# Performance work log

Measured on AMD Instinct MI355X. Metric: run time of the kernel, lower is better.

## Reference

```python
import jax, jax.numpy as jnp
import numpy as np
import math

D_MODEL = 1024
N_HEAD = 16
NUM_K = 170


def setup_inputs() -> dict:
    key = jax.random.key(0)
    ks = jax.random.split(key, 11)
    B, S, D = 2, 1024, D_MODEL
    scale = 1.0 / math.sqrt(D)
    inp = {
        "q": jax.random.normal(ks[0], (B, S, D), dtype=jnp.float32),
        "k": jax.random.normal(ks[1], (B, S, D), dtype=jnp.float32),
        "v": jax.random.normal(ks[2], (B, S, D), dtype=jnp.float32),
        # nn.Linear weights stored torch-style as (out, in); y = x @ W.T + b
        "wq": jax.random.normal(ks[3], (D, D), dtype=jnp.float32) * scale,
        "bq": jnp.zeros((D,), dtype=jnp.float32),
        "wk": jax.random.normal(ks[4], (D, D), dtype=jnp.float32) * scale,
        "bk": jnp.zeros((D,), dtype=jnp.float32),
        "wv": jax.random.normal(ks[5], (D, D), dtype=jnp.float32) * scale,
        "bv": jnp.zeros((D,), dtype=jnp.float32),
        "wo": jax.random.normal(ks[6], (D, D), dtype=jnp.float32) * scale,
        "bo": jnp.zeros((D,), dtype=jnp.float32),
    }
    return inp


def _split_heads(x):
    B, S, D = x.shape
    dh = D // N_HEAD
    return x.reshape(B, S, N_HEAD, dh).transpose(0, 2, 1, 3)  # [B,H,S,dh]


def reference(q, k, v, wq, bq, wk, bk, wv, bv, wo, bo):
    B, S, D = q.shape
    dh = D // N_HEAD
    qh = _split_heads(q @ wq.T + bq)
    kh = _split_heads(k @ wk.T + bk)
    vh = _split_heads(v @ wv.T + bv)
    # full QK^T scores [B,H,S,S]
    score = jnp.einsum("bhqd,bhkd->bhqk", qh, kh) / math.sqrt(dh)
    # topk threshold masking: keep only scores >= k-th largest per row
    num_k = min(NUM_K, S)
    topv = jax.lax.top_k(score, num_k)[0]           # [B,H,S,num_k], sorted desc
    thr = topv[..., -1:]                             # k-th largest value
    score = jnp.where(score < thr, jnp.float32(-1e18), score)
    attn = jax.nn.softmax(score, axis=-1)
    out = jnp.einsum("bhqk,bhkd->bhqd", attn, vh)   # [B,H,S,dh]
    out = out.transpose(0, 2, 1, 3).reshape(B, S, D)
    return out @ wo.T + bo
```

## Files before the change

### kernel.cpp

```cpp
#include <hip/hip_runtime.h>

typedef unsigned short u16;
typedef unsigned int   u32;
typedef short bf16x8 __attribute__((ext_vector_type(8)));
typedef float f32x4  __attribute__((ext_vector_type(4)));
typedef float f32x2  __attribute__((ext_vector_type(2)));

#define MFMA(a,b,c) __builtin_amdgcn_mfma_f32_16x16x32_bf16((a),(b),(c),0,0,0)
#define MB (1u<<20)

__device__ __forceinline__ u16 f2bf(float x) {
  u32 u = __builtin_bit_cast(u32, x);
  u32 r = (u + 0x7FFFu + ((u >> 16) & 1u)) >> 16;
  return (u16)r;
}
__device__ __forceinline__ float bf2f(u16 b) {
  u32 u = ((u32)b) << 16;
  return __builtin_bit_cast(float, u);
}
__device__ __forceinline__ void async16(void* lds, const void* g) {
  __builtin_amdgcn_global_load_lds(
      (const __attribute__((address_space(1))) u32*)g,
      (__attribute__((address_space(3))) u32*)lds, 16, 0, 0);
}


__global__ __launch_bounds__(256) void presplit_kernel(
    const float* q, const float* k, const float* v,
    const float* wq, const float* wk, const float* wv, const float* wo,
    char* ws)
{
  int y = blockIdx.y;
  const float* srcs[7] = {q, k, v, wq, wk, wv, wo};
  size_t hoffv = (y < 3) ? (size_t)y * (8*MB) : (size_t)(24*MB) + (size_t)(y-3) * (4*MB);
  size_t loffv = hoffv + ((y < 3) ? (size_t)(4*MB) : (size_t)(2*MB));
  bool wlo = (y == 0) || (y == 1) || (y == 3) || (y == 4);
  int n = (y < 3) ? (2*1024*1024) : (1024*1024);
  int idx = (blockIdx.x * 256 + threadIdx.x) * 4;
  if (idx >= n) return;
  float4 x = *(const float4*)(srcs[y] + idx);
  ushort4 hv; hv.x = f2bf(x.x); hv.y = f2bf(x.y); hv.z = f2bf(x.z); hv.w = f2bf(x.w);
  *(ushort4*)(ws + hoffv + (size_t)idx * 2) = hv;
  if (wlo) {
    ushort4 lv;
    lv.x = f2bf(x.x - bf2f(hv.x)); lv.y = f2bf(x.y - bf2f(hv.y));
    lv.z = f2bf(x.z - bf2f(hv.z)); lv.w = f2bf(x.w - bf2f(hv.w));
    *(ushort4*)(ws + loffv + (size_t)idx * 2) = lv;
  }
}

#define PA_H 0
#define PA_L 16384
#define PB_H 32768
#define PB_L 49152
#define PROJ_LDS 65536

__global__ __launch_bounds__(512, 4) void proj_kernel(char* ws,
    const float* bq, const float* bk, const float* bv)
{
  __shared__ __align__(16) char smem[PROJ_LDS];
  const int z = blockIdx.y;
  const bool split = (z < 2);
  const u16* Ah = (const u16*)(ws + (size_t)z*(8*MB));
  const u16* Al = (const u16*)(ws + (size_t)z*(8*MB) + 4*MB);
  const u16* Bh = (const u16*)(ws + (size_t)(24*MB) + (size_t)z*(4*MB));
  const u16* Bl = (const u16*)(ws + (size_t)(24*MB) + (size_t)z*(4*MB) + 2*MB);
  u16* Oh = (u16*)(ws + (size_t)(40*MB) + (size_t)z*(8*MB));
  u16* Ol = (u16*)(ws + (size_t)(40*MB) + (size_t)z*(8*MB) + 4*MB);
  const float* bias = (z == 0) ? bq : ((z == 1) ? bk : bv);
  const float scale = (z == 0) ? 0.125f : 1.0f;

  const int t = threadIdx.x, w = t >> 6, lane = t & 63;
  const int l15 = lane & 15, l4 = lane >> 4;
  const int m0 = (blockIdx.x >> 3) * 128;
  const int n0 = (blockIdx.x & 7) * 128;
  const int mw = (w >> 2) * 64, nw = (w & 3) * 32;

  f32x4 acc[4][2];
  const f32x4 z4 = {0.f, 0.f, 0.f, 0.f};
  #pragma unroll
  for (int i = 0; i < 4; ++i)
    #pragma unroll
    for (int j = 0; j < 2; ++j) acc[i][j] = z4;

  for (int kt = 0; kt < 16; ++kt) {
    __syncthreads();
    #pragma unroll
    for (int i = 0; i < 2; ++i) {
      int chunk = w*128 + i*64 + lane;
      int row = chunk >> 3, seg = chunk & 7;
      int ss = seg ^ (row & 7);
      size_t ga = (size_t)(m0 + row) * 1024 + kt*64 + ss*8;
      size_t gb = (size_t)(n0 + row) * 1024 + kt*64 + ss*8;
      async16(smem + PA_H + chunk*16, Ah + ga);
      async16(smem + PB_H + chunk*16, Bh + gb);
      if (split) {
        async16(smem + PA_L + chunk*16, Al + ga);
        async16(smem + PB_L + chunk*16, Bl + gb);
      }
    }
    __syncthreads();
    #pragma unroll
    for (int kf = 0; kf < 2; ++kf) {
      bf16x8 avh[4], avl[4], bvh[2], bvl[2];
      #pragma unroll
      for (int mf = 0; mf < 4; ++mf) {
        int row = mw + mf*16 + l15;
        int ks = kf*4 + l4;
        int off = row*128 + ((ks ^ (row & 7)) << 4);
        avh[mf] = *(const bf16x8*)(smem + PA_H + off);
        if (split) avl[mf] = *(const bf16x8*)(smem + PA_L + off);
      }
      #pragma unroll
      for (int nf = 0; nf < 2; ++nf) {
        int row = nw + nf*16 + l15;
        int ks = kf*4 + l4;
        int off = row*128 + ((ks ^ (row & 7)) << 4);
        bvh[nf] = *(const bf16x8*)(smem + PB_H + off);
        if (split) bvl[nf] = *(const bf16x8*)(smem + PB_L + off);
      }
      #pragma unroll
      for (int mf = 0; mf < 4; ++mf)
        #pragma unroll
        for (int nf = 0; nf < 2; ++nf) {
          acc[mf][nf] = MFMA(avh[mf], bvh[nf], acc[mf][nf]);
          if (split) {
            acc[mf][nf] = MFMA(avh[mf], bvl[nf], acc[mf][nf]);
            acc[mf][nf] = MFMA(avl[mf], bvh[nf], acc[mf][nf]);
          }
        }
    }
  }
  #pragma unroll
  for (int mf = 0; mf < 4; ++mf)
    #pragma unroll
    for (int nf = 0; nf < 2; ++nf) {
      int colg = n0 + nw + nf*16 + l15;
      float bb = bias[colg];
      #pragma unroll
      for (int r = 0; r < 4; ++r) {
        int rowg = m0 + mw + mf*16 + l4*4 + r;
        float val = (acc[mf][nf][r] + bb) * scale;
        u16 hb = f2bf(val);
        if (z == 2) {
          Oh[(size_t)rowg * 1024 + colg] = hb;
        } else {
          int bq_ = rowg >> 10, s = rowg & 1023;
          int hh = colg >> 6, d = colg & 63;
          int bh2 = bq_*16 + hh;
          int reg = d >> 5, l4s = (d & 31) >> 3, de = d & 7;
          int lane2 = l4s*16 + (s & 15);
          size_t o;
          if (z == 0) o = ((size_t)((bh2*64 + (s >> 4))*2 + reg))*512 + lane2*8 + de;
          else        o = ((size_t)(((bh2*8 + (s >> 7))*8 + ((s >> 4) & 7))*2 + reg))*512 + lane2*8 + de;
          Oh[o] = hb;
          Ol[o] = f2bf(val - bf2f(hb));
        }
      }
    }
}

#define FA_H 0
#define FB_H 16384
#define FIN_LDS 24576

__global__ __launch_bounds__(256, 3) void final_kernel(char* ws, const float* bo, float* out)
{
  __shared__ __align__(16) char smem[FIN_LDS];
  const u16* Ah = (const u16*)(ws + (size_t)(8*MB));
  const u16* Bh = (const u16*)(ws + (size_t)(36*MB));
  const int t = threadIdx.x, w = t >> 6, lane = t & 63;
  const int l15 = lane & 15, l4 = lane >> 4;
  const int m0 = (blockIdx.x >> 4) * 128;
  const int n0 = (blockIdx.x & 15) * 64;
  const int mw = (w >> 1) * 64, nw = (w & 1) * 32;

  f32x4 acc[4][2];
  const f32x4 z4 = {0.f, 0.f, 0.f, 0.f};
  #pragma unroll
  for (int i = 0; i < 4; ++i)
    #pragma unroll
    for (int j = 0; j < 2; ++j) acc[i][j] = z4;

  for (int kt = 0; kt < 16; ++kt) {
    __syncthreads();
    #pragma unroll
    for (int i = 0; i < 4; ++i) {
      int chunk = w*256 + i*64 + lane;
      int row = chunk >> 3, seg = chunk & 7;
      int ss = seg ^ (row & 7);
      async16(smem + FA_H + chunk*16, Ah + (size_t)(m0 + row) * 1024 + kt*64 + ss*8);
    }
    #pragma unroll
    for (int i = 0; i < 2; ++i) {
      int chunk = w*128 + i*64 + lane;
      if (chunk < 512) {
        int row = chunk >> 3, seg = chunk & 7;
        int ss = seg ^ (row & 7);
        async16(smem + FB_H + chunk*16, Bh + (size_t)(n0 + row) * 1024 + kt*64 + ss*8);
      }
    }
    __syncthreads();
    #pragma unroll
    for (int kf = 0; kf < 2; ++kf) {
      bf16x8 avh[4], bvh[2];
      #pragma unroll
      for (int mf = 0; mf < 4; ++mf) {
        int row = mw + mf*16 + l15;
        int ks = kf*4 + l4;
        avh[mf] = *(const bf16x8*)(smem + FA_H + row*128 + ((ks ^ (row & 7)) << 4));
      }
      #pragma unroll
      for (int nf = 0; nf < 2; ++nf) {
        int row = nw + nf*16 + l15;
        int ks = kf*4 + l4;
        bvh[nf] = *(const bf16x8*)(smem + FB_H + row*128 + ((ks ^ (row & 7)) << 4));
      }
      #pragma unroll
      for (int mf = 0; mf < 4; ++mf)
        #pragma unroll
        for (int nf = 0; nf < 2; ++nf)
          acc[mf][nf] = MFMA(avh[mf], bvh[nf], acc[mf][nf]);
    }
  }
  #pragma unroll
  for (int mf = 0; mf < 4; ++mf)
    #pragma unroll
    for (int nf = 0; nf < 2; ++nf) {
      int colg = n0 + nw + nf*16 + l15;
      float bb = bo[colg];
      #pragma unroll
      for (int r = 0; r < 4; ++r) {
        int rowg = m0 + mw + mf*16 + l4*4 + r;
        out[(size_t)rowg * 1024 + colg] = acc[mf][nf][r] + bb;
      }
    }
}

__global__ __launch_bounds__(256) void vtrans_kernel(char* ws)
{
  __shared__ u16 th[64][68];
  const u16* Vph = (const u16*)(ws + (size_t)(56*MB));
  u16* Vf = (u16*)(ws + 0);
  int id = blockIdx.x;
  int bh = id >> 4, sc = id & 15;
  int b = bh >> 4, h = bh & 15;
  int t = threadIdx.x;
  #pragma unroll
  for (int j = 0; j < 16; ++j) {
    int e = t + 256*j;
    int sr = e >> 6, dc = e & 63;
    th[sr][dc] = Vph[(size_t)(b*1024 + sc*64 + sr) * 1024 + h*64 + dc];
  }
  __syncthreads();
  #pragma unroll
  for (int j = 0; j < 16; ++j) {
    int e = t + 256*j;
    int dr = e >> 6, scl = e & 63;
    int s = sc*64 + scl;
    int f = dr >> 4, l15v = dr & 15;
    int half = s >> 9, ks = (s >> 5) & 15, l4v = (s >> 3) & 3, de = s & 7;
    size_t o = ((size_t)(((bh*4 + f)*2 + half)*16 + ks))*512 + (l4v*16 + l15v)*8 + de;
    Vf[o] = th[scl][dr];
  }
}

#define CB_STRIDE 528
#define CB_SZ     8448
#define P_STRIDE  2064
#define PART_OFF  33024
#define ATT_LDS   (PART_OFF + 4096)
#define KSEL 170

__global__ __launch_bounds__(512, 6) void attn_kernel(char* ws)
{
  __shared__ __align__(16) char smem[ATT_LDS];
  const u16* Qh  = (const u16*)(ws + (size_t)(40*MB));
  const u16* Ql  = (const u16*)(ws + (size_t)(44*MB));
  const u16* Kh  = (const u16*)(ws + (size_t)(48*MB));
  const u16* Kl  = (const u16*)(ws + (size_t)(52*MB));
  const u16* Vf  = (const u16*)(ws + 0);
  u16* Ath = (u16*)(ws + (size_t)(8*MB));

  int t = threadIdx.x, w = t >> 6, lane = t & 63;
  int l15 = lane & 15, l4 = lane >> 4;
  int bid = blockIdx.x;
  int logical = (bid & 7) * 256 + (bid >> 3);
  int bh = logical >> 6, qt = logical & 63;
  int b = bh >> 4, h = bh & 15;
  int q0 = qt * 16;

  const f32x4 z4 = {0.f, 0.f, 0.f, 0.f};

  bf16x8 kf[4];
#define LOADKC(KC) do { \
    size_t kb2 = ((size_t)(((bh*8 + (KC))*8 + w)*2))*512 + lane*8; \
    kf[0] = *(const bf16x8*)(Kh + kb2); \
    kf[1] = *(const bf16x8*)(Kh + kb2 + 512); \
    kf[2] = *(const bf16x8*)(Kl + kb2); \
    kf[3] = *(const bf16x8*)(Kl + kb2 + 512); \
  } while (0)

  LOADKC(0);

  bf16x8 qfh[2], qfl[2];
  {
    size_t qb2 = ((size_t)((bh*64 + qt)*2))*512 + lane*8;
    qfh[0] = *(const bf16x8*)(Qh + qb2);
    qfh[1] = *(const bf16x8*)(Qh + qb2 + 512);
    qfl[0] = *(const bf16x8*)(Ql + qb2);
    qfl[1] = *(const bf16x8*)(Ql + qb2 + 512);
  }

  f32x2 va[8], vb[8];
  #pragma unroll
  for (int kc = 0; kc < 8; ++kc) {
    f32x4 a0 = z4, a1 = z4;
    a0 = MFMA(qfh[0], kf[0], a0);
    a1 = MFMA(qfh[1], kf[1], a1);
    a0 = MFMA(qfl[0], kf[0], a0);
    a1 = MFMA(qfl[1], kf[1], a1);
    a0 = MFMA(qfh[0], kf[2], a0);
    a1 = MFMA(qfh[1], kf[3], a1);
    if (kc < 7) LOADKC(kc + 1);
    #pragma unroll
    for (int r_ = 0; r_ < 4; ++r_)
      *(float*)(smem + (kc & 1)*CB_SZ + (l4*4 + r_)*CB_STRIDE + (w*16 + l15)*4)
          = a0[r_] + a1[r_];
    asm volatile("s_waitcnt lgkmcnt(0)" ::: "memory");
    __builtin_amdgcn_s_barrier();
    asm volatile("" ::: "memory");
    va[kc] = *(const f32x2*)(smem + (kc & 1)*CB_SZ + w*CB_STRIDE + lane*8);
    vb[kc] = *(const f32x2*)(smem + (kc & 1)*CB_SZ + (w + 8)*CB_STRIDE + lane*8);
  }
  __syncthreads();

  int f = w & 3, half = w >> 2;
  size_t vbase = ((size_t)(((bh*4 + f)*2 + half)*16))*512 + lane*8;
  bf16x8 vv[2][4];
#define LOADV(BUF, G) do { \
    _Pragma("unroll") \
    for (int j_ = 0; j_ < 4; ++j_) \
      vv[BUF][j_] = *(const bf16x8*)(Vf + vbase + (size_t)((G)*4 + j_)*512); \
    } while (0)

  {
    float mA = va[0][0], mB = vb[0][0];
    #pragma unroll
    for (int i = 0; i < 8; ++i)
      #pragma unroll
      for (int e = 0; e < 2; ++e) {
        mA = fmaxf(mA, va[i][e]);
        mB = fmaxf(mB, vb[i][e]);
      }
    #pragma unroll
    for (int off = 32; off > 0; off >>= 1) {
      mA = fmaxf(mA, __shfl_xor(mA, off));
      mB = fmaxf(mB, __shfl_xor(mB, off));
    }

    float loA = mA - 16.f, hiA = mA, cLoA = 1024.f, cHiA = 1.f;
    float loB = mB - 16.f, hiB = mB, cLoB = 1024.f, cHiB = 1.f;
    float thrA = 0.f, thrB = 0.f;
    bool fA = false, fB = false;
    #pragma unroll 1
    for (int it = 0; it < 32 && !(fA && fB); ++it) {
      float gA, gB;
      if (it < 8) {
        gA = fminf(fmaxf((cLoA - (float)KSEL) / fmaxf(cLoA - cHiA, 1.f), 0.10f), 0.90f);
        gB = fminf(fmaxf((cLoB - (float)KSEL) / fmaxf(cLoB - cHiB, 1.f), 0.10f), 0.90f);
      } else {
        gA = 0.5f; gB = 0.5f;
      }
      float tA = loA + (hiA - loA) * gA;
      float tB = loB + (hiB - loB) * gB;
      if (!(tA > loA && tA < hiA)) { if (!fA) { thrA = loA; fA = true; } tA = loA; }
      if (!(tB > loB && tB < hiB)) { if (!fB) { thrB = loB; fB = true; } tB = loB; }
      int cA = 0, cB = 0;
      #pragma unroll
      for (int i = 0; i < 8; ++i)
        #pragma unroll
        for (int e = 0; e < 2; ++e) {
          cA += (int)__popcll(__ballot(va[i][e] >= tA));
          cB += (int)__popcll(__ballot(vb[i][e] >= tB));
        }
      if (!fA) {
        if (cA == KSEL) { thrA = tA; fA = true; }
        else if (cA > KSEL) { loA = tA; cLoA = (float)cA; }
        else { hiA = tA; cHiA = (float)cA; }
      }
      if (!fB) {
        if (cB == KSEL) { thrB = tB; fB = true; }
        else if (cB > KSEL) { loB = tB; cLoB = (float)cB; }
        else { hiB = tB; cHiB = (float)cB; }
      }
    }
    if (!fA) thrA = loA;
    if (!fB) thrB = loB;

    LOADV(0, 0);

    float sA = 0.f, sB = 0.f;
    #pragma unroll
    for (int i = 0; i < 8; ++i)
      #pragma unroll
      for (int e = 0; e < 2; ++e) {
        float xa = va[i][e], xb = vb[i][e];
        float ea = (xa >= thrA) ? __expf(xa - mA) : 0.f;
        float eb = (xb >= thrB) ? __expf(xb - mB) : 0.f;
        va[i][e] = ea; vb[i][e] = eb;
        sA += ea; sB += eb;
      }
    #pragma unroll
    for (int off = 32; off > 0; off >>= 1) {
      sA += __shfl_xor(sA, off);
      sB += __shfl_xor(sB, off);
    }
    float rA_ = 1.f / sA, rB_ = 1.f / sB;

    #pragma unroll
    for (int i = 0; i < 8; ++i) {
      u32 pwA = (u32)f2bf(va[i][0] * rA_) | ((u32)f2bf(va[i][1] * rA_) << 16);
      u32 pwB = (u32)f2bf(vb[i][0] * rB_) | ((u32)f2bf(vb[i][1] * rB_) << 16);
      *(u32*)(smem + w*P_STRIDE       + i*256 + lane*4) = pwA;
      *(u32*)(smem + (w + 8)*P_STRIDE + i*256 + lane*4) = pwB;
    }
  }
  __syncthreads();

  LOADV(1, 1);
  f32x4 ac0 = z4, ac1 = z4;
  #pragma unroll
  for (int g = 0; g < 4; ++g) {
    #pragma unroll
    for (int j = 0; j < 4; ++j) {
      int ksl = g*4 + j;
      bf16x8 pa = *(const bf16x8*)(smem + l15*P_STRIDE + (half*16 + ksl)*64 + l4*16);
      if (j & 1) ac1 = MFMA(pa, vv[g & 1][j], ac1);
      else       ac0 = MFMA(pa, vv[g & 1][j], ac0);
    }
    if (g == 0) LOADV(0, 2);
    if (g == 1) LOADV(1, 3);
  }
  f32x4 a = ac0 + ac1;

  if (half == 1)
    *(f32x4*)(smem + PART_OFF + (f*64 + lane)*16) = a;
  __syncthreads();
  if (half == 0) {
    f32x4 o4 = *(const f32x4*)(smem + PART_OFF + (f*64 + lane)*16);
    #pragma unroll
    for (int r = 0; r < 4; ++r) {
      float val = a[r] + o4[r];
      size_t o = (size_t)(b*1024 + q0 + l4*4 + r) * 1024 + h*64 + f*16 + l15;
      Ath[o] = f2bf(val);
    }
  }
}

extern "C" void kernel_launch(void* const* d_in, const int* in_sizes, int n_in,
                              void* d_out, int out_size, void* d_ws, size_t ws_size,
                              hipStream_t stream)
{
  const float* q  = (const float*)d_in[0];
  const float* k  = (const float*)d_in[1];
  const float* v  = (const float*)d_in[2];
  const float* wq = (const float*)d_in[3];
  const float* bq = (const float*)d_in[4];
  const float* wk = (const float*)d_in[5];
  const float* bk = (const float*)d_in[6];
  const float* wv = (const float*)d_in[7];
  const float* bv = (const float*)d_in[8];
  const float* wo = (const float*)d_in[9];
  const float* bo = (const float*)d_in[10];
  float* out = (float*)d_out;
  char* ws = (char*)d_ws;
  if (ws_size < (64ull << 20)) return;

  presplit_kernel<<<dim3(2048, 7), 256, 0, stream>>>(q, k, v, wq, wk, wv, wo, ws);
  proj_kernel<<<dim3(128, 3), 512, 0, stream>>>(ws, bq, bk, bv);
  vtrans_kernel<<<512, 256, 0, stream>>>(ws);
  attn_kernel<<<2048, 512, 0, stream>>>(ws);
  final_kernel<<<256, 256, 0, stream>>>(ws, bo, out);
}
```

Measured before the change: 138.6 us.

## Interleave projection blocks, shrink final GEMM tiles, and hoist V prefetch

The projection kernel now uses a 1D grid that interleaves the Q/K/V jobs, so the split-precision Q/K tiles and the cheaper V tiles mix across CUs. The final output GEMM switches from 128x64 to 64x64 tiles, doubling the block count to 512 to fill more CUs, at the cost of less operand reuse per block. In the attention kernel, the first two V-fragment loads are issued before the threshold search so their latency overlaps the top-k computation, which keeps more registers live.

```diff
diff --git a/kernel.cpp b/kernel.cpp
--- a/kernel.cpp
+++ b/kernel.cpp
@@ -59,7 +59,8 @@
     const float* bq, const float* bk, const float* bv)
 {
   __shared__ __align__(16) char smem[PROJ_LDS];
-  const int z = blockIdx.y;
+  const int z = blockIdx.x % 3;
+  const int tile = blockIdx.x / 3;
   const bool split = (z < 2);
   const u16* Ah = (const u16*)(ws + (size_t)z*(8*MB));
   const u16* Al = (const u16*)(ws + (size_t)z*(8*MB) + 4*MB);
@@ -72,8 +73,8 @@
 
   const int t = threadIdx.x, w = t >> 6, lane = t & 63;
   const int l15 = lane & 15, l4 = lane >> 4;
-  const int m0 = (blockIdx.x >> 3) * 128;
-  const int n0 = (blockIdx.x & 7) * 128;
+  const int m0 = (tile >> 3) * 128;
+  const int n0 = (tile & 7) * 128;
   const int mw = (w >> 2) * 64, nw = (w & 3) * 32;
 
   f32x4 acc[4][2];
@@ -160,71 +161,62 @@
     }
 }
 
-#define FA_H 0
-#define FB_H 16384
-#define FIN_LDS 24576
-
-__global__ __launch_bounds__(256, 3) void final_kernel(char* ws, const float* bo, float* out)
+#define FB_OFF 8192
+#define FIN_LDS 16384
+
+__global__ __launch_bounds__(256, 2) void final_kernel(char* ws, const float* bo, float* out)
 {
   __shared__ __align__(16) char smem[FIN_LDS];
   const u16* Ah = (const u16*)(ws + (size_t)(8*MB));
   const u16* Bh = (const u16*)(ws + (size_t)(36*MB));
   const int t = threadIdx.x, w = t >> 6, lane = t & 63;
   const int l15 = lane & 15, l4 = lane >> 4;
-  const int m0 = (blockIdx.x >> 4) * 128;
+  const int m0 = (blockIdx.x >> 4) * 64;
   const int n0 = (blockIdx.x & 15) * 64;
-  const int mw = (w >> 1) * 64, nw = (w & 1) * 32;
-
-  f32x4 acc[4][2];
+  const int mw = (w >> 1) * 32, nw = (w & 1) * 32;
+
+  f32x4 acc[2][2];
   const f32x4 z4 = {0.f, 0.f, 0.f, 0.f};
   #pragma unroll
-  for (int i = 0; i < 4; ++i)
+  for (int i = 0; i < 2; ++i)
     #pragma unroll
     for (int j = 0; j < 2; ++j) acc[i][j] = z4;
 
   for (int kt = 0; kt < 16; ++kt) {
     __syncthreads();
     #pragma unroll
-    for (int i = 0; i < 4; ++i) {
-      int chunk = w*256 + i*64 + lane;
+    for (int i = 0; i < 2; ++i) {
+      int chunk = t + i*256;
       int row = chunk >> 3, seg = chunk & 7;
       int ss = seg ^ (row & 7);
-      async16(smem + FA_H + chunk*16, Ah + (size_t)(m0 + row) * 1024 + kt*64 + ss*8);
-    }
-    #pragma unroll
-    for (int i = 0; i < 2; ++i) {
-      int chunk = w*128 + i*64 + lane;
-      if (chunk < 512) {
-        int row = chunk >> 3, seg = chunk & 7;
-        int ss = seg ^ (row & 7);
-        async16(smem + FB_H + chunk*16, Bh + (size_t)(n0 + row) * 1024 + kt*64 + ss*8);
-      }
+      async16(smem + chunk*16, Ah + (size_t)(m0 + row) * 1024 + kt*64 + ss*8);
+      async16(smem + FB_OFF + chunk*16, Bh + (size_t)(n0 + row) * 1024 + kt*64 + ss*8);
     }
     __syncthreads();
     #pragma unroll
     for (int kf = 0; kf < 2; ++kf) {
-      bf16x8 avh[4], bvh[2];
-      #pragma unroll
-      for (int mf = 0; mf < 4; ++mf) {
+      bf16x8 avh[2], bvh[2];
+      #pragma unroll
+      for (int mf = 0; mf < 2; ++mf) {
         int row = mw + mf*16 + l15;
         int ks = kf*4 + l4;
-        avh[mf] = *(const bf16x8*)(smem + FA_H + row*128 + ((ks ^ (row & 7)) << 4));
+        avh[mf] = *(const bf16x8*)(smem + row*128 + ((ks ^ (row & 7)) << 4));
       }
       #pragma unroll
       for (int nf = 0; nf < 2; ++nf) {
         int row = nw + nf*16 + l15;
         int ks = kf*4 + l4;
-        bvh[nf] = *(const bf16x8*)(smem + FB_H + row*128 + ((ks ^ (row & 7)) << 4));
-      }
-      #pragma unroll
-      for (int mf = 0; mf < 4; ++mf)
+        bvh[nf] = *(const bf16x8*)(smem + FB_OFF + row*128 + ((ks ^ (row & 7)) << 4));
+      }
+      #pragma unroll
+      for (int mf = 0; mf < 2; ++mf)
         #pragma unroll
         for (int nf = 0; nf < 2; ++nf)
           acc[mf][nf] = MFMA(avh[mf], bvh[nf], acc[mf][nf]);
     }
   }
   #pragma unroll
-  for (int mf = 0; mf < 4; ++mf)
+  for (int mf = 0; mf < 2; ++mf)
     #pragma unroll
     for (int nf = 0; nf < 2; ++nf) {
       int colg = n0 + nw + nf*16 + l15;
@@ -343,6 +335,8 @@
     for (int j_ = 0; j_ < 4; ++j_) \
       vv[BUF][j_] = *(const bf16x8*)(Vf + vbase + (size_t)((G)*4 + j_)*512); \
     } while (0)
+  LOADV(0, 0);
+  LOADV(1, 1);
 
   {
     float mA = va[0][0], mB = vb[0][0];
@@ -398,8 +392,6 @@
     if (!fA) thrA = loA;
     if (!fB) thrB = loB;
 
-    LOADV(0, 0);
-
     float sA = 0.f, sB = 0.f;
     #pragma unroll
     for (int i = 0; i < 8; ++i)
@@ -428,7 +420,6 @@
   }
   __syncthreads();
 
-  LOADV(1, 1);
   f32x4 ac0 = z4, ac1 = z4;
   #pragma unroll
   for (int g = 0; g < 4; ++g) {
@@ -478,8 +469,8 @@
   if (ws_size < (64ull << 20)) return;
 
   presplit_kernel<<<dim3(2048, 7), 256, 0, stream>>>(q, k, v, wq, wk, wv, wo, ws);
-  proj_kernel<<<dim3(128, 3), 512, 0, stream>>>(ws, bq, bk, bv);
+  proj_kernel<<<384, 512, 0, stream>>>(ws, bq, bk, bv);
   vtrans_kernel<<<512, 256, 0, stream>>>(ws);
   attn_kernel<<<2048, 512, 0, stream>>>(ws);
-  final_kernel<<<256, 256, 0, stream>>>(ws, bo, out);
-}
+  final_kernel<<<512, 256, 0, stream>>>(ws, bo, out);
+}
```

Result: slower. 146.1 us (+5.5%).
